# Performance work log

Hardware: AMD Instinct MI355X
Metric: run time of the kernel (lower is better)

The kernel has to match this reference:

```python
import jax, jax.numpy as jnp
import numpy as np

N_NODES = 100_000
N_EDGES = 1_600_000
IN_FEAT = 128
N_HEADS = 8
OUT_FEAT = 16
HF = N_HEADS * OUT_FEAT  # 128
NEG_SLOPE = 0.2


def setup_inputs() -> dict:
    key = jax.random.key(0)
    k = jax.random.split(key, 9)
    x = jax.random.normal(k[0], (N_NODES, IN_FEAT), dtype=jnp.float32)
    src = jax.random.randint(k[1], (N_EDGES,), 0, N_NODES, dtype=jnp.int64)
    dst = jax.random.randint(k[2], (N_EDGES,), 0, N_NODES, dtype=jnp.int64)
    sv = 1.0 / np.sqrt(IN_FEAT)
    sa = 1.0 / np.sqrt(HF)
    Wv = jax.random.normal(k[3], (IN_FEAT, HF), dtype=jnp.float32) * sv
    bv = jnp.zeros((HF,), dtype=jnp.float32)
    Wq = jax.random.normal(k[4], (HF, N_HEADS), dtype=jnp.float32) * sa
    bq = jnp.zeros((N_HEADS,), dtype=jnp.float32)
    Wk = jax.random.normal(k[5], (HF, N_HEADS), dtype=jnp.float32) * sa
    bk = jnp.zeros((N_HEADS,), dtype=jnp.float32)
    return {"x": x, "src": src, "dst": dst, "Wv": Wv, "bv": bv,
            "Wq": Wq, "bq": bq, "Wk": Wk, "bk": bk}


def reference(x, src, dst, Wv, bv, Wq, bq, Wk, bk):
    # Dense projections (homogeneous graph: h_src == h_dst == h)
    h = x @ Wv + bv                       # [N, H*F]
    q = h @ Wq + bq                       # [N, H]  (query, attached via dst)
    k = h @ Wk + bk                       # [N, H]  (key, attached via src)
    u = h.reshape(N_NODES, N_HEADS, OUT_FEAT)  # [N, H, F]

    # Edge scores: u_add_v('k','q') -> e_ij = k[src] + q[dst], then leaky-relu
    e = k[src] + q[dst]                   # [E, H]
    coeff = jnp.where(e >= 0, e, NEG_SLOPE * e)

    # Segment softmax over incoming edges of each destination node
    seg_max = jax.ops.segment_max(coeff, dst, num_segments=N_NODES)   # [N, H]
    ex = jnp.exp(coeff - seg_max[dst])                                # [E, H]
    denom = jax.ops.segment_sum(ex, dst, num_segments=N_NODES)       # [N, H]
    attn = ex / denom[dst]                                           # [E, H]

    # Weighted message + scatter-sum aggregate
    m = u[src] * attn[:, :, None]                                    # [E, H, F]
    v = jax.ops.segment_sum(m, dst, num_segments=N_NODES)            # [N, H, F]

    return jnp.mean(v, axis=1)                                       # [N, F]
```

## Files before the change

kernel.cpp:

```cpp
#include <hip/hip_runtime.h>
#include <hip/hip_fp16.h>

#define NFEAT 128
#define NHEADS 8
#define OUTF 16
#define NPB 256
#define MAXNB 512
#define CAP 4736

typedef _Float16 half8 __attribute__((ext_vector_type(8)));
typedef float float4v __attribute__((ext_vector_type(4)));

__global__ __launch_bounds__(256) void prep_kernel(
    const float* __restrict__ Wv, const float* __restrict__ bv,
    const float* __restrict__ Wq, const float* __restrict__ bq,
    const float* __restrict__ Wk, const float* __restrict__ bk,
    float* __restrict__ Wvq, float* __restrict__ Wvk,
    float* __restrict__ bq2, float* __restrict__ bk2)
{
    const int t = threadIdx.x;
    const int idx = blockIdx.x * 256 + t;
    const int m  = idx >> 10;
    const int j  = (idx >> 3) & 127;
    const int hd = idx & 7;
    const float* w = m ? Wk : Wq;
    float acc = 0.f;
#pragma unroll 8
    for (int c = 0; c < NFEAT; c++) acc += Wv[j * NFEAT + c] * w[c * NHEADS + hd];
    if (m) Wvk[j * NHEADS + hd] = acc;
    else   Wvq[j * NHEADS + hd] = acc;

    if (blockIdx.x == 0 && t < 16) {
        int mm = t >> 3, hh = t & 7;
        const float* ww = mm ? Wk : Wq;
        float a = mm ? bk[hh] : bq[hh];
        for (int c = 0; c < NFEAT; c++) a += bv[c] * ww[c * NHEADS + hh];
        if (mm) bk2[hh] = a;
        else    bq2[hh] = a;
    }
}

__global__ __launch_bounds__(256) void gemm_h_kernel(
    const float* __restrict__ x, const float* __restrict__ Wv,
    const float* __restrict__ bv, const float* __restrict__ Wvq,
    const float* __restrict__ Wvk, const float* __restrict__ bq2,
    const float* __restrict__ bk2, unsigned char* __restrict__ hq,
    float* __restrict__ sarr, float* __restrict__ qarr,
    float* __restrict__ karr, int M)
{
    __shared__ _Float16 sw[144][136];
    const int t = threadIdx.x;

    for (int i = t; i < 128 * 128; i += 256) {
        int k = i >> 7, n = i & 127;
        sw[n][k] = (_Float16)Wv[i];
    }
    for (int i = t; i < 128 * 16; i += 256) {
        int k = i >> 4, o = i & 15;
        float v = (o < 8) ? Wvq[k * 8 + o] : Wvk[k * 8 + (o - 8)];
        sw[128 + o][k] = (_Float16)v;
    }
    __syncthreads();

    const int wave = t >> 6, lane = t & 63;
    const int quad = lane >> 4, l16 = lane & 15;
    const int nstrips = (M + 15) >> 4;

    float bvv[8];
#pragma unroll
    for (int tl = 0; tl < 8; tl++) bvv[tl] = bv[tl * 16 + l16];
    const float qb = (l16 < 8) ? bq2[l16] : bk2[l16 - 8];

#pragma unroll
    for (int s = 0; s < 2; s++) {
        const int strip = blockIdx.x * 8 + wave + s * 4;
        if (strip >= nstrips) break;
        const int row0 = strip * 16;
        const int xr = row0 + l16;
        const bool ok = (xr < M);
        const float* xp = x + (size_t)xr * NFEAT + quad * 8;

        half8 af[4];
#pragma unroll
        for (int kc = 0; kc < 4; kc++) {
            float4 f0 = make_float4(0.f, 0.f, 0.f, 0.f);
            float4 f1 = make_float4(0.f, 0.f, 0.f, 0.f);
            if (ok) {
                f0 = *(const float4*)(xp + kc * 32);
                f1 = *(const float4*)(xp + kc * 32 + 4);
            }
            half8 a;
            a[0] = (_Float16)f0.x; a[1] = (_Float16)f0.y;
            a[2] = (_Float16)f0.z; a[3] = (_Float16)f0.w;
            a[4] = (_Float16)f1.x; a[5] = (_Float16)f1.y;
            a[6] = (_Float16)f1.z; a[7] = (_Float16)f1.w;
            af[kc] = a;
        }

        float4v acc[9];
#pragma unroll
        for (int tl = 0; tl < 9; tl++) acc[tl] = (float4v){0.f, 0.f, 0.f, 0.f};

#pragma unroll
        for (int kc = 0; kc < 4; kc++) {
#pragma unroll
            for (int tl = 0; tl < 9; tl++) {
                half8 b = *(const half8*)&sw[tl * 16 + l16][kc * 32 + quad * 8];
                acc[tl] = __builtin_amdgcn_mfma_f32_16x16x32_f16(af[kc], b, acc[tl], 0, 0, 0);
            }
        }

#pragma unroll
        for (int r = 0; r < 4; r++) {
            int row = row0 + quad * 4 + r;
            if (row < M) {
                float vv[8];
                float mx = 0.f;
#pragma unroll
                for (int tl = 0; tl < 8; tl++) {
                    vv[tl] = acc[tl][r] + bvv[tl];
                    mx = fmaxf(mx, fabsf(vv[tl]));
                }
#pragma unroll
                for (int o = 1; o <= 8; o <<= 1)
                    mx = fmaxf(mx, __shfl_xor(mx, o, 64));
                const float is = (mx > 0.f) ? 127.f / mx : 0.f;
#pragma unroll
                for (int tl = 0; tl < 8; tl++) {
                    int qi = __float2int_rn(vv[tl] * is);
                    hq[(size_t)row * NFEAT + tl * 16 + l16] = (unsigned char)(signed char)qi;
                }
                if (l16 == 0) sarr[row] = mx * (1.f / 127.f);
                float qv = acc[8][r] + qb;
                if (l16 < 8) qarr[(size_t)row * NHEADS + l16] = qv;
                else         karr[(size_t)row * NHEADS + (l16 - 8)] = qv;
            }
        }
    }
}

__global__ __launch_bounds__(1024) void bin_kernel(
    const int* __restrict__ src, const int* __restrict__ dst,
    int* __restrict__ tail, int* __restrict__ bin, int E, int NB)
{
    __shared__ int lcnt[MAXNB];
    __shared__ int lbase[MAXNB];
    const int t = threadIdx.x;
    const int e0 = blockIdx.x * 8192;

    for (int i = t; i < NB; i += 1024) lcnt[i] = 0;
    __syncthreads();

    int pack[8], bkt[8], rank[8];
#pragma unroll
    for (int k = 0; k < 8; k++) {
        int e = e0 + k * 1024 + t;
        bkt[k] = -1;
        if (e < E) {
            int d = dst[e];
            pack[k] = (src[e] << 8) | (d & (NPB - 1));
            bkt[k]  = d >> 8;
            rank[k] = atomicAdd(&lcnt[bkt[k]], 1);
        }
    }
    __syncthreads();
    for (int i = t; i < NB; i += 1024)
        lbase[i] = lcnt[i] ? atomicAdd(&tail[i], lcnt[i]) : 0;
    __syncthreads();

#pragma unroll
    for (int k = 0; k < 8; k++) {
        if (bkt[k] >= 0) {
            int pos = lbase[bkt[k]] + rank[k];
            if (pos < CAP) bin[(size_t)bkt[k] * CAP + pos] = pack[k];
        }
    }
}

__global__ __launch_bounds__(1024) void bucket_build_kernel(
    const int* __restrict__ bin, const int* __restrict__ tail,
    int* __restrict__ deg, int* __restrict__ off,
    int* __restrict__ csr, int N, int NB)
{
    __shared__ int stail[MAXNB];
    __shared__ int lcnt[NPB];
    __shared__ int lcur[NPB];
    __shared__ int lcsr[CAP];

    const int b = blockIdx.x;
    const int t = threadIdx.x;

    for (int i = t; i < MAXNB; i += 1024) stail[i] = (i < NB) ? tail[i] : 0;
    if (t < NPB) lcnt[t] = 0;
    __syncthreads();

    for (int o = 1; o < MAXNB; o <<= 1) {
        int u = (t < MAXNB && t >= o) ? stail[t - o] : 0;
        __syncthreads();
        if (t < MAXNB) stail[t] += u;
        __syncthreads();
    }
    const int gbase = (b > 0) ? stail[b - 1] : 0;
    const int cnt = min(tail[b], CAP);
    const int n0 = b << 8;
    const int* mybin = bin + (size_t)b * CAP;

    for (int i = t; i < cnt; i += 1024) atomicAdd(&lcnt[mybin[i] & (NPB - 1)], 1);
    __syncthreads();

    if (t < NPB) lcur[t] = lcnt[t];
    __syncthreads();
    for (int o = 1; o < NPB; o <<= 1) {
        int u = (t < NPB && t >= o) ? lcur[t - o] : 0;
        __syncthreads();
        if (t < NPB) lcur[t] += u;
        __syncthreads();
    }
    if (t < NPB) {
        int excl = lcur[t] - lcnt[t];
        lcur[t] = excl;
        int node = n0 + t;
        if (node < N) {
            deg[node] = lcnt[t];
            off[node] = gbase + excl;
        }
    }
    __syncthreads();

    for (int i = t; i < cnt; i += 1024) {
        int p = mybin[i];
        int r = atomicAdd(&lcur[p & (NPB - 1)], 1);
        lcsr[r] = p >> 8;
    }
    __syncthreads();

    for (int i = t; i < cnt; i += 1024) csr[gbase + i] = lcsr[i];
}

__global__ __launch_bounds__(256) void agg_kernel(
    const int* __restrict__ csr, const int* __restrict__ off,
    const int* __restrict__ deg, const float* __restrict__ karr,
    const float* __restrict__ qarr, const unsigned char* __restrict__ hq,
    const float* __restrict__ sarr, float* __restrict__ out, int nnodes)
{
    const int g = threadIdx.x >> 3;
    const int j = threadIdx.x & 7;
    const int d = blockIdx.x * 32 + g;
    if (d >= nnodes) return;

    const int dg = deg[d];
    const int o0 = off[d];
    const float q1 = qarr[d * NHEADS + j];
    const unsigned char* hb = hq + j * 16;

    float acc[16];
#pragma unroll
    for (int i = 0; i < 16; i++) acc[i] = 0.f;
    float den = 0.f;

    for (int e = 0; e < dg; e += 8) {
        const int rem = dg - e;
        int s[8];
        s[0] = csr[o0 + e];
#pragma unroll
        for (int k = 1; k < 8; k++) s[k] = (rem > k) ? csr[o0 + e + k] : s[0];

        int4  r[8];
        float kv[8];
        float sc[8];
#pragma unroll
        for (int k = 0; k < 8; k++) {
            r[k]  = *(const int4*)(hb + (size_t)s[k] * NFEAT);
            kv[k] = karr[s[k] * NHEADS + j];
            sc[k] = sarr[s[k]];
        }

#pragma unroll
        for (int k = 0; k < 8; k++) {
            float c = kv[k] + q1;
            c = fmaxf(c, 0.2f * c);
            const float p = (rem > k) ? __expf(c) * 0.0009765625f : 0.f;
            den += p;
            const float w = p * sc[k];
            const int4 rv = r[k];
            const int d0 = rv.x, d1 = rv.y, d2 = rv.z, d3 = rv.w;
            acc[0]  = fmaf(w, (float)(signed char)(d0      ), acc[0]);
            acc[1]  = fmaf(w, (float)(signed char)(d0 >>  8), acc[1]);
            acc[2]  = fmaf(w, (float)(signed char)(d0 >> 16), acc[2]);
            acc[3]  = fmaf(w, (float)(d0 >> 24),              acc[3]);
            acc[4]  = fmaf(w, (float)(signed char)(d1      ), acc[4]);
            acc[5]  = fmaf(w, (float)(signed char)(d1 >>  8), acc[5]);
            acc[6]  = fmaf(w, (float)(signed char)(d1 >> 16), acc[6]);
            acc[7]  = fmaf(w, (float)(d1 >> 24),              acc[7]);
            acc[8]  = fmaf(w, (float)(signed char)(d2      ), acc[8]);
            acc[9]  = fmaf(w, (float)(signed char)(d2 >>  8), acc[9]);
            acc[10] = fmaf(w, (float)(signed char)(d2 >> 16), acc[10]);
            acc[11] = fmaf(w, (float)(d2 >> 24),              acc[11]);
            acc[12] = fmaf(w, (float)(signed char)(d3      ), acc[12]);
            acc[13] = fmaf(w, (float)(signed char)(d3 >>  8), acc[13]);
            acc[14] = fmaf(w, (float)(signed char)(d3 >> 16), acc[14]);
            acc[15] = fmaf(w, (float)(d3 >> 24),              acc[15]);
        }
    }

    const float inv = (dg > 0) ? 0.125f / den : 0.f;
    float f[16];
#pragma unroll
    for (int i = 0; i < 16; i++) f[i] = acc[i] * inv;

#pragma unroll
    for (int o = 1; o <= 4; o <<= 1)
#pragma unroll
        for (int i = 0; i < 16; i++) f[i] += __shfl_xor(f[i], o, 64);

    if (j == 0) {
        float4* o4 = (float4*)(out + (size_t)d * OUTF);
        o4[0] = make_float4(f[0],  f[1],  f[2],  f[3]);
        o4[1] = make_float4(f[4],  f[5],  f[6],  f[7]);
        o4[2] = make_float4(f[8],  f[9],  f[10], f[11]);
        o4[3] = make_float4(f[12], f[13], f[14], f[15]);
    }
}

extern "C" void kernel_launch(void* const* d_in, const int* in_sizes, int n_in,
                              void* d_out, int out_size, void* d_ws, size_t ws_size,
                              hipStream_t stream)
{
    const float* x   = (const float*)d_in[0];
    const int*   src = (const int*)d_in[1];
    const int*   dst = (const int*)d_in[2];
    const float* Wv  = (const float*)d_in[3];
    const float* bv  = (const float*)d_in[4];
    const float* Wq  = (const float*)d_in[5];
    const float* bq  = (const float*)d_in[6];
    const float* Wk  = (const float*)d_in[7];
    const float* bk  = (const float*)d_in[8];
    float* out = (float*)d_out;

    const int N = in_sizes[0] / NFEAT;
    const int E = in_sizes[1];
    const int NB = (N + NPB - 1) / NPB;

    unsigned char* hq = (unsigned char*)d_ws;
    float* sarr = (float*)(hq + (size_t)N * NFEAT);
    float* qarr = sarr + N;
    float* karr = qarr + (size_t)N * NHEADS;
    int* deg    = (int*)(karr + (size_t)N * NHEADS);
    int* off    = deg + N;
    int* csr    = off + N;
    float* Wvq  = (float*)(csr + E);
    float* Wvk  = Wvq + NFEAT * NHEADS;
    float* bq2  = Wvk + NFEAT * NHEADS;
    float* bk2  = bq2 + NHEADS;
    int* tail   = (int*)(bk2 + NHEADS);
    int* bin    = tail + MAXNB;

    hipMemsetAsync(tail, 0, MAXNB * sizeof(int), stream);

    prep_kernel<<<dim3(8), dim3(256), 0, stream>>>(Wv, bv, Wq, bq, Wk, bk,
                                                   Wvq, Wvk, bq2, bk2);

    bin_kernel<<<dim3((E + 8191) / 8192), dim3(1024), 0, stream>>>(
        src, dst, tail, bin, E, NB);

    bucket_build_kernel<<<dim3(NB), dim3(1024), 0, stream>>>(
        bin, tail, deg, off, csr, N, NB);

    const int nstrips = (N + 15) / 16;
    gemm_h_kernel<<<dim3((nstrips + 7) / 8), dim3(256), 0, stream>>>(
        x, Wv, bv, Wvq, Wvk, bq2, bk2, hq, sarr, qarr, karr, N);

    agg_kernel<<<dim3((N + 31) / 32), dim3(256), 0, stream>>>(
        csr, off, deg, karr, qarr, hq, sarr, out, N);
}
```

Baseline: 211.3 us.

## Pretranspose fp16 weights in prep, widen GEMM strips, split agg edges across 16 lanes

The prep kernel now writes a transposed fp16 weight matrix (Wv plus the fused q/k columns), so each GEMM block loads shared memory with vectorized copies instead of converting and transposing per block. GEMM blocks process 16 strips instead of 8, halving the number of weight loads. The aggregation kernel assigns 16 lanes per destination node, each half handling 4 edges per step with a vectorized int4 CSR index load and clamped source indices, plus an extra shuffle stage to combine halves. The int4 CSR read past a node's segment relies on clamping and alignment and may read beyond the csr buffer end for the last nodes.

```diff
diff --git a/kernel.cpp b/kernel.cpp
--- a/kernel.cpp
+++ b/kernel.cpp
@@ -15,8 +15,7 @@
     const float* __restrict__ Wv, const float* __restrict__ bv,
     const float* __restrict__ Wq, const float* __restrict__ bq,
     const float* __restrict__ Wk, const float* __restrict__ bk,
-    float* __restrict__ Wvq, float* __restrict__ Wvk,
-    float* __restrict__ bq2, float* __restrict__ bk2)
+    _Float16* __restrict__ Wt, float* __restrict__ bq2, float* __restrict__ bk2)
 {
     const int t = threadIdx.x;
     const int idx = blockIdx.x * 256 + t;
@@ -27,8 +26,16 @@
     float acc = 0.f;
 #pragma unroll 8
     for (int c = 0; c < NFEAT; c++) acc += Wv[j * NFEAT + c] * w[c * NHEADS + hd];
-    if (m) Wvk[j * NHEADS + hd] = acc;
-    else   Wvq[j * NHEADS + hd] = acc;
+    Wt[(128 + (m << 3) + hd) * 128 + j] = (_Float16)acc;
+
+    {
+        const int n  = idx >> 4;
+        const int k0 = (idx & 15) << 3;
+        half8 v;
+#pragma unroll
+        for (int u = 0; u < 8; u++) v[u] = (_Float16)Wv[(k0 + u) * NFEAT + n];
+        *(half8*)&Wt[n * 128 + k0] = v;
+    }
 
     if (blockIdx.x == 0 && t < 16) {
         int mm = t >> 3, hh = t & 7;
@@ -41,9 +48,8 @@
 }
 
 __global__ __launch_bounds__(256) void gemm_h_kernel(
-    const float* __restrict__ x, const float* __restrict__ Wv,
-    const float* __restrict__ bv, const float* __restrict__ Wvq,
-    const float* __restrict__ Wvk, const float* __restrict__ bq2,
+    const float* __restrict__ x, const _Float16* __restrict__ Wt,
+    const float* __restrict__ bv, const float* __restrict__ bq2,
     const float* __restrict__ bk2, unsigned char* __restrict__ hq,
     float* __restrict__ sarr, float* __restrict__ qarr,
     float* __restrict__ karr, int M)
@@ -51,14 +57,12 @@
     __shared__ _Float16 sw[144][136];
     const int t = threadIdx.x;
 
-    for (int i = t; i < 128 * 128; i += 256) {
-        int k = i >> 7, n = i & 127;
-        sw[n][k] = (_Float16)Wv[i];
-    }
-    for (int i = t; i < 128 * 16; i += 256) {
-        int k = i >> 4, o = i & 15;
-        float v = (o < 8) ? Wvq[k * 8 + o] : Wvk[k * 8 + (o - 8)];
-        sw[128 + o][k] = (_Float16)v;
+    {
+        const uint4* Wt4 = (const uint4*)Wt;
+        for (int i = t; i < 144 * 16; i += 256) {
+            int col = i >> 4, c8 = (i & 15) << 3;
+            *(uint4*)&sw[col][c8] = Wt4[i];
+        }
     }
     __syncthreads();
 
@@ -72,8 +76,8 @@
     const float qb = (l16 < 8) ? bq2[l16] : bk2[l16 - 8];
 
 #pragma unroll
-    for (int s = 0; s < 2; s++) {
-        const int strip = blockIdx.x * 8 + wave + s * 4;
+    for (int s = 0; s < 4; s++) {
+        const int strip = blockIdx.x * 16 + wave + s * 4;
         if (strip >= nstrips) break;
         const int row0 = strip * 16;
         const int xr = row0 + l16;
@@ -237,53 +241,52 @@
     for (int i = t; i < cnt; i += 1024) csr[gbase + i] = lcsr[i];
 }
 
-__global__ __launch_bounds__(256) void agg_kernel(
+__global__ __launch_bounds__(256, 8) void agg_kernel(
     const int* __restrict__ csr, const int* __restrict__ off,
     const int* __restrict__ deg, const float* __restrict__ karr,
     const float* __restrict__ qarr, const unsigned char* __restrict__ hq,
     const float* __restrict__ sarr, float* __restrict__ out, int nnodes)
 {
-    const int g = threadIdx.x >> 3;
-    const int j = threadIdx.x & 7;
-    const int d = blockIdx.x * 32 + g;
+    const int g = threadIdx.x >> 4;
+    const int jj = threadIdx.x & 15;
+    const int j = jj & 7;
+    const int half = jj >> 3;
+    const int d = blockIdx.x * 16 + g;
     if (d >= nnodes) return;
 
     const int dg = deg[d];
     const int o0 = off[d];
     const float q1 = qarr[d * NHEADS + j];
     const unsigned char* hb = hq + j * 16;
+    const int nmax = nnodes - 1;
 
     float acc[16];
 #pragma unroll
     for (int i = 0; i < 16; i++) acc[i] = 0.f;
     float den = 0.f;
 
-    for (int e = 0; e < dg; e += 8) {
-        const int rem = dg - e;
-        int s[8];
-        s[0] = csr[o0 + e];
-#pragma unroll
-        for (int k = 1; k < 8; k++) s[k] = (rem > k) ? csr[o0 + e + k] : s[0];
-
-        int4  r[8];
-        float kv[8];
-        float sc[8];
-#pragma unroll
-        for (int k = 0; k < 8; k++) {
+    for (int e0 = 0; e0 < dg; e0 += 8) {
+        const int eb = e0 + half * 4;
+        int4 s4 = *(const int4*)(csr + o0 + eb);
+        int s[4] = { s4.x, s4.y, s4.z, s4.w };
+        int4 r[4];
+        float kv[4], sc[4];
+#pragma unroll
+        for (int k = 0; k < 4; k++) {
+            s[k]  = min(max(s[k], 0), nmax);
             r[k]  = *(const int4*)(hb + (size_t)s[k] * NFEAT);
             kv[k] = karr[s[k] * NHEADS + j];
             sc[k] = sarr[s[k]];
         }
 
 #pragma unroll
-        for (int k = 0; k < 8; k++) {
+        for (int k = 0; k < 4; k++) {
             float c = kv[k] + q1;
             c = fmaxf(c, 0.2f * c);
-            const float p = (rem > k) ? __expf(c) * 0.0009765625f : 0.f;
+            const float p = (eb + k < dg) ? __expf(c) * 0.0009765625f : 0.f;
             den += p;
             const float w = p * sc[k];
-            const int4 rv = r[k];
-            const int d0 = rv.x, d1 = rv.y, d2 = rv.z, d3 = rv.w;
+            const int d0 = r[k].x, d1 = r[k].y, d2 = r[k].z, d3 = r[k].w;
             acc[0]  = fmaf(w, (float)(signed char)(d0      ), acc[0]);
             acc[1]  = fmaf(w, (float)(signed char)(d0 >>  8), acc[1]);
             acc[2]  = fmaf(w, (float)(signed char)(d0 >> 16), acc[2]);
@@ -303,17 +306,18 @@
         }
     }
 
+    den += __shfl_xor(den, 8, 64);
     const float inv = (dg > 0) ? 0.125f / den : 0.f;
     float f[16];
 #pragma unroll
     for (int i = 0; i < 16; i++) f[i] = acc[i] * inv;
 
 #pragma unroll
-    for (int o = 1; o <= 4; o <<= 1)
+    for (int o = 1; o <= 8; o <<= 1)
 #pragma unroll
         for (int i = 0; i < 16; i++) f[i] += __shfl_xor(f[i], o, 64);
 
-    if (j == 0) {
+    if (jj == 0) {
         float4* o4 = (float4*)(out + (size_t)d * OUTF);
         o4[0] = make_float4(f[0],  f[1],  f[2],  f[3]);
         o4[1] = make_float4(f[4],  f[5],  f[6],  f[7]);
@@ -348,9 +352,8 @@
     int* deg    = (int*)(karr + (size_t)N * NHEADS);
     int* off    = deg + N;
     int* csr    = off + N;
-    float* Wvq  = (float*)(csr + E);
-    float* Wvk  = Wvq + NFEAT * NHEADS;
-    float* bq2  = Wvk + NFEAT * NHEADS;
+    _Float16* Wt = (_Float16*)(csr + E);
+    float* bq2  = (float*)(Wt + 144 * 128);
     float* bk2  = bq2 + NHEADS;
     int* tail   = (int*)(bk2 + NHEADS);
     int* bin    = tail + MAXNB;
@@ -358,7 +361,7 @@
     hipMemsetAsync(tail, 0, MAXNB * sizeof(int), stream);
 
     prep_kernel<<<dim3(8), dim3(256), 0, stream>>>(Wv, bv, Wq, bq, Wk, bk,
-                                                   Wvq, Wvk, bq2, bk2);
+                                                   Wt, bq2, bk2);
 
     bin_kernel<<<dim3((E + 8191) / 8192), dim3(1024), 0, stream>>>(
         src, dst, tail, bin, E, NB);
@@ -367,9 +370,9 @@
         bin, tail, deg, off, csr, N, NB);
 
     const int nstrips = (N + 15) / 16;
-    gemm_h_kernel<<<dim3((nstrips + 7) / 8), dim3(256), 0, stream>>>(
-        x, Wv, bv, Wvq, Wvk, bq2, bk2, hq, sarr, qarr, karr, N);
-
-    agg_kernel<<<dim3((N + 31) / 32), dim3(256), 0, stream>>>(
+    gemm_h_kernel<<<dim3((nstrips + 15) / 16), dim3(256), 0, stream>>>(
+        x, Wt, bv, bq2, bk2, hq, sarr, qarr, karr, N);
+
+    agg_kernel<<<dim3((N + 15) / 16), dim3(256), 0, stream>>>(
         csr, off, deg, karr, qarr, hq, sarr, out, N);
 }
```

Result: slower. 230.0 us (+8.9%).
